# Performance work log

Hardware: AMD Instinct MI355X
Metric: run time of the kernel (lower is better)

## Reference

```python
import jax, jax.numpy as jnp
import numpy as np

DECAY = 0.9      # LIF membrane decay per step
V_TH = 1.0       # spike threshold


def setup_inputs() -> dict:
    key = jax.random.key(0)
    k1, k2, k3, k4, k5 = jax.random.split(key, 5)
    B, D, N = 256, 1024, 2048
    density = 0.3
    external_inputs = jax.random.normal(k1, (B, D), dtype=jnp.float32)
    # nn.Linear(input_dim, num_neurons): weight [N, D], bias [N]
    W_in = jax.random.normal(k2, (N, D), dtype=jnp.float32) / np.sqrt(D)
    b_in = jnp.zeros((N,), dtype=jnp.float32)
    adj_weights = jax.random.normal(k3, (N, N), dtype=jnp.float32) * 0.01
    mask = (jax.random.uniform(k4, (N, N)) < density).astype(jnp.float32)
    mask = mask * (1.0 - jnp.eye(N, dtype=jnp.float32))  # zero diagonal
    return {
        "external_inputs": external_inputs,
        "W_in": W_in,
        "b_in": b_in,
        "adj_weights": adj_weights,
        "mask": mask,
        "time_steps": 64,
    }


def _spike(x):
    # Heaviside spike: 1 if membrane exceeds threshold
    return (x >= 0.0).astype(x.dtype)


def reference(external_inputs, W_in, b_in, adj_weights, mask, time_steps):
    B = external_inputs.shape[0]
    N = adj_weights.shape[0]
    I_ext = external_inputs @ W_in.T + b_in              # [B, N]
    W_eff = adj_weights * mask                           # [N, N]
    V0 = jnp.zeros((B, N), dtype=external_inputs.dtype)
    s0 = jnp.zeros((B, N), dtype=external_inputs.dtype)

    def step(carry, _):
        V, s = carry
        I_total = I_ext + s @ W_eff.T                    # recurrent current
        V = DECAY * V + I_total                          # LIF integration
        s_new = _spike(V - V_TH)
        V = V * (1.0 - s_new)                            # reset on spike
        return (V, s_new), s_new

    (_, _), spike_hist = jax.lax.scan(step, (V0, s0), None, length=time_steps)
    return spike_hist.mean(axis=0)                       # [B, N] firing rates
```

## Files before the change

### kernel.cpp

```cpp
#include <hip/hip_runtime.h>
#include <cstdint>
#include <cstddef>

#define N_NEU 2048
#define D_IN  1024
#define T_STEPS 64

typedef _Float16 f16x8 __attribute__((ext_vector_type(8)));
typedef _Float16 f16x4 __attribute__((ext_vector_type(4)));
typedef float    f32x4 __attribute__((ext_vector_type(4)));
typedef unsigned u32x4 __attribute__((ext_vector_type(4)));

#define MFMA16(a, b, c) __builtin_amdgcn_mfma_f32_16x16x32_f16((a), (b), (c), 0, 0, 0)


__device__ inline f16x8 expand8(unsigned b) {
  u32x4 t;
  t[0] = ((b & 1u)   ? 0x3C00u : 0u) | ((b & 2u)   ? 0x3C000000u : 0u);
  t[1] = ((b & 4u)   ? 0x3C00u : 0u) | ((b & 8u)   ? 0x3C000000u : 0u);
  t[2] = ((b & 16u)  ? 0x3C00u : 0u) | ((b & 32u)  ? 0x3C000000u : 0u);
  t[3] = ((b & 64u)  ? 0x3C00u : 0u) | ((b & 128u) ? 0x3C000000u : 0u);
  return __builtin_bit_cast(f16x8, t);
}

__global__ __launch_bounds__(256) void k_wsplit(const float* __restrict__ adj,
                                                const float* __restrict__ mask,
                                                _Float16* __restrict__ Wh,
                                                _Float16* __restrict__ Wl,
                                                unsigned long long* __restrict__ bmv) {
  const int idx = blockIdx.x * 256 + threadIdx.x;
  if (idx < 2 * 256 * 64) bmv[idx] = 0ull;
  const int total4 = (N_NEU * N_NEU) / 4;
  for (int i = idx; i < total4; i += gridDim.x * 256) {
    float4 a = ((const float4*)adj)[i];
    float4 m = ((const float4*)mask)[i];
    float w0 = a.x * m.x, w1 = a.y * m.y, w2 = a.z * m.z, w3 = a.w * m.w;
    f16x4 h, lo;
    h[0] = (_Float16)w0; lo[0] = (_Float16)((w0 - (float)h[0]) * 4096.0f);
    h[1] = (_Float16)w1; lo[1] = (_Float16)((w1 - (float)h[1]) * 4096.0f);
    h[2] = (_Float16)w2; lo[2] = (_Float16)((w2 - (float)h[2]) * 4096.0f);
    h[3] = (_Float16)w3; lo[3] = (_Float16)((w3 - (float)h[3]) * 4096.0f);
    ((f16x4*)Wh)[i] = h;
    ((f16x4*)Wl)[i] = lo;
  }
}

__global__ __launch_bounds__(256) void k_iext(const float* __restrict__ ext,
                                              const float* __restrict__ Win,
                                              const float* __restrict__ bin,
                                              float* __restrict__ Iext) {
  __shared__ float At[32][68];
  __shared__ float Bt[32][68];
  const int tid = threadIdx.x;
  const int b0 = (blockIdx.x & 3) * 64;
  const int n0 = (blockIdx.x >> 2) * 64;
  const int tx = tid & 15, ty = tid >> 4;
  float acc[4][4] = {};
  for (int kt = 0; kt < D_IN / 32; ++kt) {
    const int k0 = kt * 32;
#pragma unroll
    for (int i = 0; i < 8; ++i) {
      int e = tid + i * 256;
      int kk = e & 31, row = e >> 5;
      At[kk][row] = ext[(size_t)(b0 + row) * D_IN + k0 + kk];
      Bt[kk][row] = Win[(size_t)(n0 + row) * D_IN + k0 + kk];
    }
    __syncthreads();
    for (int kk = 0; kk < 32; ++kk) {
      f32x4 a = *(const f32x4*)&At[kk][ty * 4];
      f32x4 b = *(const f32x4*)&Bt[kk][tx * 4];
#pragma unroll
      for (int i = 0; i < 4; ++i)
#pragma unroll
        for (int j = 0; j < 4; ++j) acc[i][j] += a[i] * b[j];
    }
    __syncthreads();
  }
#pragma unroll
  for (int i = 0; i < 4; ++i)
#pragma unroll
    for (int j = 0; j < 4; ++j)
      Iext[(size_t)(b0 + ty * 4 + i) * N_NEU + n0 + tx * 4 + j] = acc[i][j] + bin[n0 + tx * 4 + j];
}

__global__ __launch_bounds__(512, 2) void k_fused8(
    const _Float16* __restrict__ Wh, const _Float16* __restrict__ Wl,
    const float* __restrict__ Iext, unsigned long long* __restrict__ bmv,
    float* __restrict__ out) {
  __shared__ float red[4 * 32 * 32];
  __shared__ unsigned bmA[32 * 64];
  __shared__ unsigned bmB[32 * 64];

  const int tid = threadIdx.x;
  const int lane = tid & 63;
  const int kw = tid >> 6;
  const int l15 = lane & 15;
  const int klo = lane >> 4;
  const int sh = klo * 8;
  const int gp = blockIdx.x >> 6;
  const int ns = blockIdx.x & 63;
  const int n0 = ns * 32;
  const int gA = gp, gB = gp + 4;
  const float inv4096 = 1.0f / 4096.0f;
  const f32x4 z4 = {0.f, 0.f, 0.f, 0.f};

  float IxA[2], IxB[2];
#pragma unroll
  for (int j = 0; j < 2; ++j) {
    IxA[j] = Iext[(size_t)(gA * 32 + j * 16 + (tid >> 5)) * N_NEU + n0 + (tid & 31)];
    IxB[j] = Iext[(size_t)(gB * 32 + j * 16 + (tid >> 5)) * N_NEU + n0 + (tid & 31)];
  }

  const _Float16* whb = Wh + (size_t)(n0 + l15) * N_NEU + kw * 256 + klo * 8;
  const _Float16* wlb = Wl + (size_t)(n0 + l15) * N_NEU + kw * 256 + klo * 8;
  f16x8 whf[2][8], wlf[2][8];
#pragma unroll
  for (int nt = 0; nt < 2; ++nt)
#pragma unroll
    for (int kcl = 0; kcl < 8; ++kcl) {
      whf[nt][kcl] = *(const f16x8*)(whb + nt * 16 * N_NEU + kcl * 32);
      wlf[nt][kcl] = *(const f16x8*)(wlb + nt * 16 * N_NEU + kcl * 32);
    }

  float VA[2] = {0.f, 0.f}, VB[2] = {0.f, 0.f};
  unsigned cA[2] = {0u, 0u}, cB[2] = {0u, 0u};
  unsigned long long vA[4], vB[4];

  auto spec_issue = [&](int g, int buf, unsigned long long (&v)[4]) {
    const unsigned long long* src = bmv + (size_t)buf * 16384 + (size_t)g * 2048 + tid;
#pragma unroll
    for (int i = 0; i < 4; ++i)
      v[i] = __hip_atomic_load(src + (size_t)i * 512, __ATOMIC_RELAXED, __HIP_MEMORY_SCOPE_AGENT);
  };
  auto check_retry = [&](int g, int buf, unsigned want, unsigned long long (&v)[4]) {
    const unsigned long long* src = bmv + (size_t)buf * 16384 + (size_t)g * 2048 + tid;
    unsigned need = 0u;
#pragma unroll
    for (int i = 0; i < 4; ++i)
      if ((unsigned)(v[i] >> 32) != want) need |= 1u << i;
    while (need) {
      __builtin_amdgcn_s_sleep(2);
#pragma unroll
      for (int i = 0; i < 4; ++i)
        if (need & (1u << i)) {
          v[i] = __hip_atomic_load(src + (size_t)i * 512,
                                   __ATOMIC_RELAXED, __HIP_MEMORY_SCOPE_AGENT);
          if ((unsigned)(v[i] >> 32) == want) need &= ~(1u << i);
        }
    }
  };
  auto stage = [&](unsigned* bm, const unsigned long long (&v)[4]) {
#pragma unroll
    for (int i = 0; i < 4; ++i) {
      const int w = i * 512 + tid, r = w >> 6, nsw = w & 63;
      bm[r * 64 + (nsw ^ ((r & 15) << 2))] = (unsigned)v[i];
    }
  };
  auto gemm = [&](const unsigned* bm, float (&cI)[2]) {
    f32x4 acch[2][2], accl[2][2];
#pragma unroll
    for (int mt = 0; mt < 2; ++mt)
#pragma unroll
      for (int nt = 0; nt < 2; ++nt) { acch[mt][nt] = z4; accl[mt][nt] = z4; }
#pragma unroll
    for (int mt = 0; mt < 2; ++mt) {
      const int row = mt * 16 + l15;
      const int swz = l15 << 2;
      const u32x4 q0 = *(const u32x4*)&bm[row * 64 + ((kw * 8) ^ swz)];
      const u32x4 q1 = *(const u32x4*)&bm[row * 64 + (((kw * 8) | 4) ^ swz)];
#pragma unroll
      for (int kcl = 0; kcl < 8; ++kcl) {
        const unsigned word = (kcl < 4) ? q0[kcl] : q1[kcl - 4];
        const f16x8 a = expand8((word >> sh) & 0xFFu);
        acch[mt][0] = MFMA16(a, whf[0][kcl], acch[mt][0]);
        accl[mt][0] = MFMA16(a, wlf[0][kcl], accl[mt][0]);
        acch[mt][1] = MFMA16(a, whf[1][kcl], acch[mt][1]);
        accl[mt][1] = MFMA16(a, wlf[1][kcl], accl[mt][1]);
      }
    }
    f32x4 cb[2][2];
#pragma unroll
    for (int mt = 0; mt < 2; ++mt)
#pragma unroll
      for (int nt = 0; nt < 2; ++nt) cb[mt][nt] = acch[mt][nt] + accl[mt][nt] * inv4096;
    const int cbn = lane & 15, rq = (lane >> 4) << 2;
    if (kw >= 4) {
      const int p = kw - 4;
#pragma unroll
      for (int mt = 0; mt < 2; ++mt)
#pragma unroll
        for (int nt = 0; nt < 2; ++nt) {
          const int col = nt * 16 + cbn;
          const int r0 = (mt * 16 + rq) ^ ((col & 7) << 2);
          *(f32x4*)(red + (p * 32 + col) * 32 + r0) = cb[mt][nt];
        }
    }
    __syncthreads();
    if (kw < 4) {
#pragma unroll
      for (int mt = 0; mt < 2; ++mt)
#pragma unroll
        for (int nt = 0; nt < 2; ++nt) {
          const int col = nt * 16 + cbn;
          const int r0 = (mt * 16 + rq) ^ ((col & 7) << 2);
          float* p2 = red + (kw * 32 + col) * 32 + r0;
          f32x4 o = *(const f32x4*)p2;
          o += cb[mt][nt];
          *(f32x4*)p2 = o;
        }
    }
    __syncthreads();
#pragma unroll
    for (int j = 0; j < 2; ++j) {
      const int o = j * 512 + tid;
      const int row = o >> 5, col = o & 31;
      const int rs = row ^ ((col & 7) << 2);
      float s = 0.0f;
#pragma unroll
      for (int p = 0; p < 4; ++p) s += red[(p * 32 + col) * 32 + rs];
      cI[j] = s;
    }
  };
  auto lif = [&](const float (&cI)[2], const float (&Ix)[2], float (&V)[2],
                 unsigned (&cnt)[2], int g, int nbuf, unsigned tag, bool dostore) {
#pragma unroll
    for (int j = 0; j < 2; ++j) {
      float I = cI[j] + Ix[j];
      float v = 0.9f * V[j] + I;
      bool sp = (v - 1.0f) >= 0.0f;
      V[j] = sp ? 0.0f : v;
      cnt[j] += sp ? 1u : 0u;
      if (dostore) {
        unsigned long long ba = __ballot(sp);
        const int rowf = g * 32 + j * 16 + kw * 2;
        const unsigned long long tg = ((unsigned long long)tag) << 32;
        if (lane == 0)
          __hip_atomic_store(bmv + (size_t)nbuf * 16384 + (size_t)rowf * 64 + ns,
                             tg | (unsigned)ba, __ATOMIC_RELAXED, __HIP_MEMORY_SCOPE_AGENT);
        else if (lane == 32)
          __hip_atomic_store(bmv + (size_t)nbuf * 16384 + (size_t)(rowf + 1) * 64 + ns,
                             tg | (unsigned)(ba >> 32), __ATOMIC_RELAXED, __HIP_MEMORY_SCOPE_AGENT);
      }
    }
  };

  {
    const float cz[2] = {0.f, 0.f};
    lif(cz, IxA, VA, cA, gA, 1, 1u, true);
    lif(cz, IxB, VB, cB, gB, 1, 1u, true);
    spec_issue(gA, 1, vA);
  }

  for (int t = 1; t < T_STEPS; ++t) {
    const int cbuf = t & 1, nbuf = (t + 1) & 1;
    const bool last = (t == T_STEPS - 1);
    float cI[2];

    check_retry(gA, cbuf, (unsigned)t, vA);
    stage(bmA, vA);
    __syncthreads();
    spec_issue(gB, cbuf, vB);
    gemm(bmA, cI);
    lif(cI, IxA, VA, cA, gA, nbuf, (unsigned)(t + 1), !last);

    check_retry(gB, cbuf, (unsigned)t, vB);
    stage(bmB, vB);
    __syncthreads();
    if (!last) spec_issue(gA, nbuf, vA);
    gemm(bmB, cI);
    lif(cI, IxB, VB, cB, gB, nbuf, (unsigned)(t + 1), !last);
  }

#pragma unroll
  for (int j = 0; j < 2; ++j) {
    const int rA = gA * 32 + j * 16 + (tid >> 5);
    const int rB = gB * 32 + j * 16 + (tid >> 5);
    out[(size_t)rA * N_NEU + n0 + (tid & 31)] = (float)cA[j] * 0.015625f;
    out[(size_t)rB * N_NEU + n0 + (tid & 31)] = (float)cB[j] * 0.015625f;
  }
}

extern "C" void kernel_launch(void* const* d_in, const int* in_sizes, int n_in,
                              void* d_out, int out_size, void* d_ws, size_t ws_size,
                              hipStream_t stream) {
  (void)in_sizes; (void)n_in; (void)out_size; (void)ws_size;
  const float* ext  = (const float*)d_in[0];
  const float* Win  = (const float*)d_in[1];
  const float* bin  = (const float*)d_in[2];
  const float* adj  = (const float*)d_in[3];
  const float* mask = (const float*)d_in[4];
  unsigned char* ws = (unsigned char*)d_ws;

  _Float16* Wh   = (_Float16*)(ws);
  _Float16* Wl   = (_Float16*)(ws + (size_t)(8u << 20));
  float*    Iext = (float*)   (ws + (size_t)(16u << 20));
  unsigned long long* bmv = (unsigned long long*)(ws + (size_t)(18u << 20));
  float* out = (float*)d_out;

  hipLaunchKernelGGL(k_wsplit, dim3(2048), dim3(256), 0, stream, adj, mask, Wh, Wl, bmv);
  hipLaunchKernelGGL(k_iext,   dim3(128),  dim3(256), 0, stream, ext, Win, bin, Iext);
  hipLaunchKernelGGL(k_fused8, dim3(256),  dim3(512), 0, stream,
                     Wh, Wl, Iext, bmv, out);
}
```

Measured before the change: 443.9 us.

## Double block to 1024 threads, splitting K across 16 waves

Each fused recurrent block now runs 16 waves instead of 8, so every wave handles 128 of the K dimension instead of 256 and keeps half as many fp16 weight fragments in registers. The cross-wave reduction buffer doubles to 8 partial slices and each thread owns one output neuron instead of two. The goal is more waves hiding MFMA, LDS and polling latency in the serial time-step loop, at the cost of a larger LDS reduction and more threads taking part in each barrier. The launch_bounds hint of 4 blocks per CU at 1024 threads cannot be met, and the grid and synchronisation scheme are unchanged.

```diff
diff --git a/kernel.cpp b/kernel.cpp
--- a/kernel.cpp
+++ b/kernel.cpp
@@ -83,11 +83,11 @@
       Iext[(size_t)(b0 + ty * 4 + i) * N_NEU + n0 + tx * 4 + j] = acc[i][j] + bin[n0 + tx * 4 + j];
 }
 
-__global__ __launch_bounds__(512, 2) void k_fused8(
+__global__ __launch_bounds__(1024, 4) void k_fused9(
     const _Float16* __restrict__ Wh, const _Float16* __restrict__ Wl,
     const float* __restrict__ Iext, unsigned long long* __restrict__ bmv,
     float* __restrict__ out) {
-  __shared__ float red[4 * 32 * 32];
+  __shared__ float red[8 * 32 * 32];
   __shared__ unsigned bmA[32 * 64];
   __shared__ unsigned bmB[32 * 64];
 
@@ -101,62 +101,59 @@
   const int ns = blockIdx.x & 63;
   const int n0 = ns * 32;
   const int gA = gp, gB = gp + 4;
+  const int orow = tid >> 5, ocol = tid & 31;
   const float inv4096 = 1.0f / 4096.0f;
   const f32x4 z4 = {0.f, 0.f, 0.f, 0.f};
 
-  float IxA[2], IxB[2];
-#pragma unroll
-  for (int j = 0; j < 2; ++j) {
-    IxA[j] = Iext[(size_t)(gA * 32 + j * 16 + (tid >> 5)) * N_NEU + n0 + (tid & 31)];
-    IxB[j] = Iext[(size_t)(gB * 32 + j * 16 + (tid >> 5)) * N_NEU + n0 + (tid & 31)];
-  }
-
-  const _Float16* whb = Wh + (size_t)(n0 + l15) * N_NEU + kw * 256 + klo * 8;
-  const _Float16* wlb = Wl + (size_t)(n0 + l15) * N_NEU + kw * 256 + klo * 8;
-  f16x8 whf[2][8], wlf[2][8];
+  const float IxA = Iext[(size_t)(gA * 32 + orow) * N_NEU + n0 + ocol];
+  const float IxB = Iext[(size_t)(gB * 32 + orow) * N_NEU + n0 + ocol];
+
+  const _Float16* whb = Wh + (size_t)(n0 + l15) * N_NEU + kw * 128 + klo * 8;
+  const _Float16* wlb = Wl + (size_t)(n0 + l15) * N_NEU + kw * 128 + klo * 8;
+  f16x8 whf[2][4], wlf[2][4];
 #pragma unroll
   for (int nt = 0; nt < 2; ++nt)
 #pragma unroll
-    for (int kcl = 0; kcl < 8; ++kcl) {
+    for (int kcl = 0; kcl < 4; ++kcl) {
       whf[nt][kcl] = *(const f16x8*)(whb + nt * 16 * N_NEU + kcl * 32);
       wlf[nt][kcl] = *(const f16x8*)(wlb + nt * 16 * N_NEU + kcl * 32);
     }
 
-  float VA[2] = {0.f, 0.f}, VB[2] = {0.f, 0.f};
-  unsigned cA[2] = {0u, 0u}, cB[2] = {0u, 0u};
-  unsigned long long vA[4], vB[4];
-
-  auto spec_issue = [&](int g, int buf, unsigned long long (&v)[4]) {
+  float VA = 0.f, VB = 0.f;
+  unsigned cntA = 0u, cntB = 0u;
+  unsigned long long vA[2], vB[2];
+
+  auto spec_issue = [&](int g, int buf, unsigned long long (&v)[2]) {
     const unsigned long long* src = bmv + (size_t)buf * 16384 + (size_t)g * 2048 + tid;
 #pragma unroll
-    for (int i = 0; i < 4; ++i)
-      v[i] = __hip_atomic_load(src + (size_t)i * 512, __ATOMIC_RELAXED, __HIP_MEMORY_SCOPE_AGENT);
-  };
-  auto check_retry = [&](int g, int buf, unsigned want, unsigned long long (&v)[4]) {
+    for (int i = 0; i < 2; ++i)
+      v[i] = __hip_atomic_load(src + (size_t)i * 1024, __ATOMIC_RELAXED, __HIP_MEMORY_SCOPE_AGENT);
+  };
+  auto check_retry = [&](int g, int buf, unsigned want, unsigned long long (&v)[2]) {
     const unsigned long long* src = bmv + (size_t)buf * 16384 + (size_t)g * 2048 + tid;
     unsigned need = 0u;
 #pragma unroll
-    for (int i = 0; i < 4; ++i)
+    for (int i = 0; i < 2; ++i)
       if ((unsigned)(v[i] >> 32) != want) need |= 1u << i;
     while (need) {
       __builtin_amdgcn_s_sleep(2);
 #pragma unroll
-      for (int i = 0; i < 4; ++i)
+      for (int i = 0; i < 2; ++i)
         if (need & (1u << i)) {
-          v[i] = __hip_atomic_load(src + (size_t)i * 512,
+          v[i] = __hip_atomic_load(src + (size_t)i * 1024,
                                    __ATOMIC_RELAXED, __HIP_MEMORY_SCOPE_AGENT);
           if ((unsigned)(v[i] >> 32) == want) need &= ~(1u << i);
         }
     }
   };
-  auto stage = [&](unsigned* bm, const unsigned long long (&v)[4]) {
-#pragma unroll
-    for (int i = 0; i < 4; ++i) {
-      const int w = i * 512 + tid, r = w >> 6, nsw = w & 63;
+  auto stage = [&](unsigned* bm, const unsigned long long (&v)[2]) {
+#pragma unroll
+    for (int i = 0; i < 2; ++i) {
+      const int w = i * 1024 + tid, r = w >> 6, nsw = w & 63;
       bm[r * 64 + (nsw ^ ((r & 15) << 2))] = (unsigned)v[i];
     }
   };
-  auto gemm = [&](const unsigned* bm, float (&cI)[2]) {
+  auto gemm = [&](const unsigned* bm, float& cI_out) {
     f32x4 acch[2][2], accl[2][2];
 #pragma unroll
     for (int mt = 0; mt < 2; ++mt)
@@ -166,37 +163,34 @@
     for (int mt = 0; mt < 2; ++mt) {
       const int row = mt * 16 + l15;
       const int swz = l15 << 2;
-      const u32x4 q0 = *(const u32x4*)&bm[row * 64 + ((kw * 8) ^ swz)];
-      const u32x4 q1 = *(const u32x4*)&bm[row * 64 + (((kw * 8) | 4) ^ swz)];
-#pragma unroll
-      for (int kcl = 0; kcl < 8; ++kcl) {
-        const unsigned word = (kcl < 4) ? q0[kcl] : q1[kcl - 4];
-        const f16x8 a = expand8((word >> sh) & 0xFFu);
+      const u32x4 q = *(const u32x4*)&bm[row * 64 + ((kw * 4) ^ swz)];
+#pragma unroll
+      for (int kcl = 0; kcl < 4; ++kcl) {
+        const f16x8 a = expand8((q[kcl] >> sh) & 0xFFu);
         acch[mt][0] = MFMA16(a, whf[0][kcl], acch[mt][0]);
         accl[mt][0] = MFMA16(a, wlf[0][kcl], accl[mt][0]);
         acch[mt][1] = MFMA16(a, whf[1][kcl], acch[mt][1]);
         accl[mt][1] = MFMA16(a, wlf[1][kcl], accl[mt][1]);
       }
     }
-    f32x4 cb[2][2];
 #pragma unroll
     for (int mt = 0; mt < 2; ++mt)
 #pragma unroll
-      for (int nt = 0; nt < 2; ++nt) cb[mt][nt] = acch[mt][nt] + accl[mt][nt] * inv4096;
+      for (int nt = 0; nt < 2; ++nt) acch[mt][nt] += accl[mt][nt] * inv4096;
     const int cbn = lane & 15, rq = (lane >> 4) << 2;
-    if (kw >= 4) {
-      const int p = kw - 4;
+    if (kw >= 8) {
+      const int p = kw - 8;
 #pragma unroll
       for (int mt = 0; mt < 2; ++mt)
 #pragma unroll
         for (int nt = 0; nt < 2; ++nt) {
           const int col = nt * 16 + cbn;
           const int r0 = (mt * 16 + rq) ^ ((col & 7) << 2);
-          *(f32x4*)(red + (p * 32 + col) * 32 + r0) = cb[mt][nt];
+          *(f32x4*)(red + (p * 32 + col) * 32 + r0) = acch[mt][nt];
         }
     }
     __syncthreads();
-    if (kw < 4) {
+    if (kw < 8) {
 #pragma unroll
       for (int mt = 0; mt < 2; ++mt)
 #pragma unroll
@@ -205,79 +199,63 @@
           const int r0 = (mt * 16 + rq) ^ ((col & 7) << 2);
           float* p2 = red + (kw * 32 + col) * 32 + r0;
           f32x4 o = *(const f32x4*)p2;
-          o += cb[mt][nt];
+          o += acch[mt][nt];
           *(f32x4*)p2 = o;
         }
     }
     __syncthreads();
-#pragma unroll
-    for (int j = 0; j < 2; ++j) {
-      const int o = j * 512 + tid;
-      const int row = o >> 5, col = o & 31;
-      const int rs = row ^ ((col & 7) << 2);
-      float s = 0.0f;
-#pragma unroll
-      for (int p = 0; p < 4; ++p) s += red[(p * 32 + col) * 32 + rs];
-      cI[j] = s;
-    }
-  };
-  auto lif = [&](const float (&cI)[2], const float (&Ix)[2], float (&V)[2],
-                 unsigned (&cnt)[2], int g, int nbuf, unsigned tag, bool dostore) {
-#pragma unroll
-    for (int j = 0; j < 2; ++j) {
-      float I = cI[j] + Ix[j];
-      float v = 0.9f * V[j] + I;
-      bool sp = (v - 1.0f) >= 0.0f;
-      V[j] = sp ? 0.0f : v;
-      cnt[j] += sp ? 1u : 0u;
-      if (dostore) {
-        unsigned long long ba = __ballot(sp);
-        const int rowf = g * 32 + j * 16 + kw * 2;
-        const unsigned long long tg = ((unsigned long long)tag) << 32;
-        if (lane == 0)
-          __hip_atomic_store(bmv + (size_t)nbuf * 16384 + (size_t)rowf * 64 + ns,
-                             tg | (unsigned)ba, __ATOMIC_RELAXED, __HIP_MEMORY_SCOPE_AGENT);
-        else if (lane == 32)
-          __hip_atomic_store(bmv + (size_t)nbuf * 16384 + (size_t)(rowf + 1) * 64 + ns,
-                             tg | (unsigned)(ba >> 32), __ATOMIC_RELAXED, __HIP_MEMORY_SCOPE_AGENT);
-      }
-    }
-  };
-
-  {
-    const float cz[2] = {0.f, 0.f};
-    lif(cz, IxA, VA, cA, gA, 1, 1u, true);
-    lif(cz, IxB, VB, cB, gB, 1, 1u, true);
-    spec_issue(gA, 1, vA);
-  }
+    const int rs = orow ^ ((ocol & 7) << 2);
+    float s = 0.0f;
+#pragma unroll
+    for (int p = 0; p < 8; ++p) s += red[(p * 32 + ocol) * 32 + rs];
+    cI_out = s;
+  };
+  auto lif = [&](float cI, float Ix, float& V, unsigned& cnt, int g, int nbuf,
+                 unsigned tag, bool dostore) {
+    float I = cI + Ix;
+    float v = 0.9f * V + I;
+    bool sp = (v - 1.0f) >= 0.0f;
+    V = sp ? 0.0f : v;
+    cnt += sp ? 1u : 0u;
+    if (dostore) {
+      unsigned long long ba = __ballot(sp);
+      const int rowf = g * 32 + kw * 2;
+      const unsigned long long tg = ((unsigned long long)tag) << 32;
+      if (lane == 0)
+        __hip_atomic_store(bmv + (size_t)nbuf * 16384 + (size_t)rowf * 64 + ns,
+                           tg | (unsigned)ba, __ATOMIC_RELAXED, __HIP_MEMORY_SCOPE_AGENT);
+      else if (lane == 32)
+        __hip_atomic_store(bmv + (size_t)nbuf * 16384 + (size_t)(rowf + 1) * 64 + ns,
+                           tg | (unsigned)(ba >> 32), __ATOMIC_RELAXED, __HIP_MEMORY_SCOPE_AGENT);
+    }
+  };
+
+  lif(0.0f, IxA, VA, cntA, gA, 1, 1u, true);
+  lif(0.0f, IxB, VB, cntB, gB, 1, 1u, true);
+  spec_issue(gA, 1, vA);
 
   for (int t = 1; t < T_STEPS; ++t) {
     const int cbuf = t & 1, nbuf = (t + 1) & 1;
     const bool last = (t == T_STEPS - 1);
-    float cI[2];
+    float cI;
 
     check_retry(gA, cbuf, (unsigned)t, vA);
     stage(bmA, vA);
     __syncthreads();
     spec_issue(gB, cbuf, vB);
     gemm(bmA, cI);
-    lif(cI, IxA, VA, cA, gA, nbuf, (unsigned)(t + 1), !last);
+    lif(cI, IxA, VA, cntA, gA, nbuf, (unsigned)(t + 1), !last);
 
     check_retry(gB, cbuf, (unsigned)t, vB);
     stage(bmB, vB);
     __syncthreads();
     if (!last) spec_issue(gA, nbuf, vA);
     gemm(bmB, cI);
-    lif(cI, IxB, VB, cB, gB, nbuf, (unsigned)(t + 1), !last);
+    lif(cI, IxB, VB, cntB, gB, nbuf, (unsigned)(t + 1), !last);
   }
 
-#pragma unroll
-  for (int j = 0; j < 2; ++j) {
-    const int rA = gA * 32 + j * 16 + (tid >> 5);
-    const int rB = gB * 32 + j * 16 + (tid >> 5);
-    out[(size_t)rA * N_NEU + n0 + (tid & 31)] = (float)cA[j] * 0.015625f;
-    out[(size_t)rB * N_NEU + n0 + (tid & 31)] = (float)cB[j] * 0.015625f;
-  }
+  out[(size_t)(gA * 32 + orow) * N_NEU + n0 + ocol] = (float)cntA * 0.015625f;
+  out[(size_t)(gB * 32 + orow) * N_NEU + n0 + ocol] = (float)cntB * 0.015625f;
 }
 
 extern "C" void kernel_launch(void* const* d_in, const int* in_sizes, int n_in,
@@ -299,6 +277,6 @@
 
   hipLaunchKernelGGL(k_wsplit, dim3(2048), dim3(256), 0, stream, adj, mask, Wh, Wl, bmv);
   hipLaunchKernelGGL(k_iext,   dim3(128),  dim3(256), 0, stream, ext, Win, bin, Iext);
-  hipLaunchKernelGGL(k_fused8, dim3(256),  dim3(512), 0, stream,
+  hipLaunchKernelGGL(k_fused9, dim3(256),  dim3(1024), 0, stream,
                      Wh, Wl, Iext, bmv, out);
 }
```

Measured after the change: 649.2 us. 46.2% more time.
